# Kernel optimization log

Measured on AMD Instinct MI355X. Metric: run time of the kernel, lower is better.

The kernel has to match this reference:

```python
import jax, jax.numpy as jnp
import numpy as np

ALPHA = 0.5  # mixing weight between dot-product and wedge-norm terms


def setup_inputs() -> dict:
    key = jax.random.key(0)
    kq, kk, kv = jax.random.split(key, 3)
    B, L, H, E = 2, 2048, 8, 32
    queries = jax.random.normal(kq, (B, L, H, E), dtype=jnp.float32)
    keys = jax.random.normal(kk, (B, L, H, E), dtype=jnp.float32)
    values = jax.random.normal(kv, (B, L, H, E), dtype=jnp.float32)
    return {"queries": queries, "keys": keys, "values": values}


def reference(queries, keys, values):
    # queries: [B,L,H,E], keys: [B,S,H,E], values: [B,S,H,D]
    E = queries.shape[-1]
    scale = 1.0 / jnp.sqrt(jnp.asarray(E, dtype=queries.dtype))
    # dot product scores: [B,H,L,S]
    dot = jnp.einsum('blhe,bshe->bhls', queries, keys)
    # squared norms -> broadcastable [B,H,L,1] and [B,H,1,S]
    qn2 = jnp.sum(queries ** 2, axis=-1).transpose(0, 2, 1)[..., :, None]
    kn2 = jnp.sum(keys ** 2, axis=-1).transpose(0, 2, 1)[..., None, :]
    # wedge (Clifford) squared norm, clamped at 0
    wedge = jax.nn.relu(qn2 * kn2 - dot ** 2)
    scores = (ALPHA * dot - (1.0 - ALPHA) * wedge) * scale
    attn = jax.nn.softmax(scores, axis=-1)  # [B,H,L,S]
    # out: [B,L,H,D]
    out = jnp.einsum('bhls,bshd->blhd', attn, values)
    return out
```

## Files before the change

kernel.cpp:

```cpp
#include <hip/hip_runtime.h>
#include <hip/hip_bf16.h>
#include <math.h>


#define NB 2
#define NL 2048
#define NS 2048
#define NH 8
#define NBH 16
#define CSC 0.12751742f

#define WS_KN2_OFF 0u
#define WS_KHKL_OFF 131072u
#define WS_VT_OFF (131072u + 4194304u)
#define WS_PACC_OFF (131072u + 4194304u + 2097152u)
#define WS_PML_OFF (WS_PACC_OFF + 16777216u)
#define WS_NEED (WS_PML_OFF + 1048576u)

typedef float f32x4 __attribute__((ext_vector_type(4)));
typedef short s16x8 __attribute__((ext_vector_type(8)));
typedef unsigned short u16;

__device__ inline unsigned pk2(float a, float b) {
    __hip_bfloat162 t = __float22bfloat162_rn(make_float2(a, b));
    union { __hip_bfloat162 h; unsigned u; } cv;
    cv.h = t;
    return cv.u;
}
template <int CTRL>
__device__ inline float dpp_add(float x) {
    return x + __int_as_float(__builtin_amdgcn_mov_dpp(__float_as_int(x), CTRL, 0xF, 0xF, false));
}
__device__ inline void dma16(const void* gp, void* lp) {
    __builtin_amdgcn_global_load_lds(
        (__attribute__((address_space(1))) void*)(void*)gp,
        (__attribute__((address_space(3))) void*)lp, 16, 0, 0);
}
__device__ inline int swzK(int row) { return (row ^ (row >> 2)) & 3; }
__device__ inline int swzV(int row) { return (row + (row >> 3)) & 7; }

__global__ __launch_bounds__(256) void ga_pre(const float* __restrict__ K,
                                              const float* __restrict__ V,
                                              float* __restrict__ kn2w,
                                              u16* __restrict__ khkl,
                                              u16* __restrict__ vtw) {
    __shared__ float Vf[64][36];
    const int T = threadIdx.x;
    const int bh = blockIdx.x >> 5, stile = blockIdx.x & 31;
    const int b = bh >> 3, h = bh & 7;
    const int s0 = stile * 64;
    const int sk = T >> 2, kc = T & 3;

    const float* kp = K + ((size_t)((b * NS + s0 + sk) * NH + h)) * 32 + kc * 8;
    float4 f0 = *(const float4*)kp, f1 = *(const float4*)(kp + 4);
    float kx[8] = {f0.x, f0.y, f0.z, f0.w, f1.x, f1.y, f1.z, f1.w};
    unsigned hh[4], ll[4];
    float kn2p = 0.f;
#pragma unroll
    for (int i = 0; i < 4; i++) {
        float x0 = kx[2 * i], x1 = kx[2 * i + 1];
        kn2p = fmaf(x0, x0, kn2p);
        kn2p = fmaf(x1, x1, kn2p);
        unsigned h01 = pk2(x0, x1);
        hh[i] = h01;
        float h0 = __uint_as_float(h01 << 16);
        float h1 = __uint_as_float(h01 & 0xffff0000u);
        ll[i] = pk2(x0 - h0, x1 - h1);
    }
    u16* kd = khkl + ((size_t)(bh * NS + s0 + sk)) * 64;
    const int swk = sk & 7;
    *(uint4*)(kd + ((kc ^ swk) * 8)) = make_uint4(hh[0], hh[1], hh[2], hh[3]);
    *(uint4*)(kd + (((4 + kc) ^ swk) * 8)) = make_uint4(ll[0], ll[1], ll[2], ll[3]);
    kn2p = dpp_add<0xB1>(kn2p);
    kn2p = dpp_add<0x4E>(kn2p);
    if (kc == 0) kn2w[bh * NS + s0 + sk] = kn2p;

    const float* vp = V + ((size_t)((b * NS + s0 + sk) * NH + h)) * 32 + kc * 8;
    float4 g0 = *(const float4*)vp, g1 = *(const float4*)(vp + 4);
    *(float4*)&Vf[sk][kc * 8] = g0;
    *(float4*)&Vf[sk][kc * 8 + 4] = g1;
    __syncthreads();
    const int dr = T >> 3, c = T & 7;
    float vv[8];
#pragma unroll
    for (int i = 0; i < 8; i++) vv[i] = Vf[c * 8 + i][dr];
    const int phys = c ^ (dr & 7);
    *(uint4*)(vtw + ((size_t)(bh * 32 + dr)) * NS + s0 + phys * 8) =
        make_uint4(pk2(vv[0], vv[1]), pk2(vv[2], vv[3]), pk2(vv[4], vv[5]), pk2(vv[6], vv[7]));
}

__global__ __launch_bounds__(256, 4) void ga_dma(
    const float* __restrict__ Q, const float* __restrict__ kn2w,
    const u16* __restrict__ khkl, const u16* __restrict__ vtw,
    float* __restrict__ pacc, float* __restrict__ pml) {
    __shared__ u16 sK[2][64][64];
    __shared__ u16 sV[2][32][64];
    __shared__ u16 sP[4][16][64];

    const int T = threadIdx.x;
    const int lane = T & 63, wave = T >> 6;
    const int g = lane >> 4, lc = lane & 15, g8 = g * 8;
    const int blk = blockIdx.x;
    const int qt = blk & 31, strip = (blk >> 5) & 3, bh = blk >> 7;
    const int b = bh >> 3, h = bh & 7;
    const int qw = qt * 64 + wave * 16;
    const int kb0 = strip * 512;

    const float* qrow = Q + ((size_t)((b * NL + qw + lc) * NH + h)) * 32 + g8;
    float4 qa = *(const float4*)qrow, qb = *(const float4*)(qrow + 4);
    float q8[8] = {qa.x, qa.y, qa.z, qa.w, qb.x, qb.y, qb.z, qb.w};
    union { unsigned u4[4]; s16x8 v; } qh_, ql_;
    float qn2 = 0.f;
#pragma unroll
    for (int i = 0; i < 4; i++) {
        float x0 = q8[2 * i], x1 = q8[2 * i + 1];
        qn2 = fmaf(x0, x0, qn2);
        qn2 = fmaf(x1, x1, qn2);
        unsigned h01 = pk2(x0, x1);
        qh_.u4[i] = h01;
        float h0 = __uint_as_float(h01 << 16);
        float h1 = __uint_as_float(h01 & 0xffff0000u);
        ql_.u4[i] = pk2(x0 - h0, x1 - h1);
    }
    const s16x8 qh = qh_.v, ql = ql_.v;
    qn2 += __shfl_xor(qn2, 16);
    qn2 += __shfl_xor(qn2, 32);

    const char* ksrc = (const char*)khkl +
        ((size_t)(bh * NS + kb0 + 16 * wave)) * 128 + lane * 16;
    const char* vsrc = (const char*)vtw +
        ((size_t)(bh * 32 + 8 * wave + (lane >> 3))) * (NS * 2) +
        (size_t)(kb0 + (lane & 7) * 8) * 2;
    const float* kn2b = kn2w + (size_t)bh * NS + kb0;

    dma16(ksrc, &sK[0][16 * wave][0]);
    dma16(ksrc + 1024, &sK[0][16 * wave + 8][0]);
    dma16(vsrc, &sV[0][8 * wave][0]);
    __syncthreads();

    s16x8 ones;
#pragma unroll
    for (int i = 0; i < 8; i++) ones[i] = (short)0x3F80;

    f32x4 acc0 = {0.f, 0.f, 0.f, 0.f}, acc1 = {0.f, 0.f, 0.f, 0.f};
    float m = -1e30f, l = 0.f;
    const f32x4 z = {0.f, 0.f, 0.f, 0.f};
    const int sw = lc & 7;

    for (int t = 0; t < 8; ++t) {
        const int cur = t & 1;
        if (t + 1 < 8) {
            const char* k2 = ksrc + (size_t)(t + 1) * 8192;
            const char* v2 = vsrc + (size_t)(t + 1) * 128;
            dma16(k2, &sK[cur ^ 1][16 * wave][0]);
            dma16(k2 + 1024, &sK[cur ^ 1][16 * wave + 8][0]);
            dma16(v2, &sV[cur ^ 1][8 * wave][0]);
        }
        const int kl64 = t * 64;

        f32x4 d[4], kn2v[4];
#pragma unroll
        for (int st = 0; st < 4; st++) {
            kn2v[st] = *(const f32x4*)(kn2b + kl64 + 16 * st + 4 * g);
            s16x8 kh = *(s16x8*)&sK[cur][16 * st + lc][(g ^ sw) * 8];
            s16x8 klo = *(s16x8*)&sK[cur][16 * st + lc][((4 + g) ^ sw) * 8];
            f32x4 dd = __builtin_amdgcn_mfma_f32_16x16x32_bf16(klo, qh, z, 0, 0, 0);
            dd = __builtin_amdgcn_mfma_f32_16x16x32_bf16(kh, ql, dd, 0, 0, 0);
            dd = __builtin_amdgcn_mfma_f32_16x16x32_bf16(kh, qh, dd, 0, 0, 0);
            d[st] = dd;
        }
        s16x8 va0 = *(s16x8*)&sV[cur][lc][(g ^ sw) * 8];
        s16x8 va1 = *(s16x8*)&sV[cur][lc][((4 + g) ^ sw) * 8];
        s16x8 va2 = *(s16x8*)&sV[cur][lc + 16][(g ^ sw) * 8];
        s16x8 va3 = *(s16x8*)&sV[cur][lc + 16][((4 + g) ^ sw) * 8];

        float sc[4][4];
#pragma unroll
        for (int st = 0; st < 4; st++)
#pragma unroll
            for (int r = 0; r < 4; r++) {
                float dd = d[st][r];
                float c = qn2 * kn2v[st][r];
                sc[st][r] = fminf(dd, fmaf(dd, dd, -c) + dd);
            }

        float x0 = fmaxf(fmaxf(sc[0][0], sc[0][1]), fmaxf(sc[0][2], sc[0][3]));
        float x1 = fmaxf(fmaxf(sc[1][0], sc[1][1]), fmaxf(sc[1][2], sc[1][3]));
        float x2 = fmaxf(fmaxf(sc[2][0], sc[2][1]), fmaxf(sc[2][2], sc[2][3]));
        float x3 = fmaxf(fmaxf(sc[3][0], sc[3][1]), fmaxf(sc[3][2], sc[3][3]));
        float tm = fmaxf(fmaxf(x0, x1), fmaxf(x2, x3));
        tm = fmaxf(tm, __shfl_xor(tm, 16));
        tm = fmaxf(tm, __shfl_xor(tm, 32));
        const float nm = fmaxf(m, tm);
        const float negmC = -nm * CSC;
        const float al = __builtin_amdgcn_exp2f(fmaf(m, CSC, negmC));
        m = nm;
        float p[4][4];
#pragma unroll
        for (int st = 0; st < 4; st++)
#pragma unroll
            for (int r = 0; r < 4; r++)
                p[st][r] = __builtin_amdgcn_exp2f(fmaf(sc[st][r], CSC, negmC));

#pragma unroll
        for (int st = 0; st < 4; st++) {
            const int off = (((2 * st + (g >> 1)) ^ sw) << 3) + ((g & 1) << 2);
            *(uint2*)&sP[wave][lc][off] =
                make_uint2(pk2(p[st][0], p[st][1]), pk2(p[st][2], p[st][3]));
        }
        __builtin_amdgcn_s_waitcnt(0xC07F);
        s16x8 pb0 = *(s16x8*)&sP[wave][lc][(g ^ sw) * 8];
        s16x8 pb1 = *(s16x8*)&sP[wave][lc][((4 + g) ^ sw) * 8];

        acc0 *= al;
        acc1 *= al;
        acc0 = __builtin_amdgcn_mfma_f32_16x16x32_bf16(va0, pb0, acc0, 0, 0, 0);
        acc0 = __builtin_amdgcn_mfma_f32_16x16x32_bf16(va1, pb1, acc0, 0, 0, 0);
        acc1 = __builtin_amdgcn_mfma_f32_16x16x32_bf16(va2, pb0, acc1, 0, 0, 0);
        acc1 = __builtin_amdgcn_mfma_f32_16x16x32_bf16(va3, pb1, acc1, 0, 0, 0);
        f32x4 lt = __builtin_amdgcn_mfma_f32_16x16x32_bf16(ones, pb0, z, 0, 0, 0);
        lt = __builtin_amdgcn_mfma_f32_16x16x32_bf16(ones, pb1, lt, 0, 0, 0);
        l = fmaf(l, al, lt[0]);

        __syncthreads();
    }

    float* pa = pacc + (((size_t)bh * 4 + strip) * NL + (qw + lc)) * 32;
    *(f32x4*)(pa + 4 * g) = acc0;
    *(f32x4*)(pa + 16 + 4 * g) = acc1;
    if (g == 0) {
        *(float2*)(pml + (((size_t)bh * 4 + strip) * NL + (qw + lc)) * 2) =
            make_float2(m, l);
    }
}

__global__ __launch_bounds__(256) void ga_combine(const float* __restrict__ pacc,
                                                  const float* __restrict__ pml,
                                                  float* __restrict__ O) {
    const int tid = blockIdx.x * 256 + threadIdx.x;
    const int dq = tid & 7, q = (tid >> 3) & 2047, bh = tid >> 14;
    const int b = bh >> 3, h = bh & 7;
    float m[4], l[4];
#pragma unroll
    for (int s = 0; s < 4; s++) {
        float2 t = *(const float2*)(pml + (((size_t)bh * 4 + s) * NL + q) * 2);
        m[s] = t.x;
        l[s] = t.y;
    }
    float mf = fmaxf(fmaxf(m[0], m[1]), fmaxf(m[2], m[3]));
    float w[4], L = 0.f;
#pragma unroll
    for (int s = 0; s < 4; s++) {
        w[s] = __builtin_amdgcn_exp2f((m[s] - mf) * CSC);
        L = fmaf(l[s], w[s], L);
    }
    const float inv = 1.f / L;
    float4 o = make_float4(0.f, 0.f, 0.f, 0.f);
#pragma unroll
    for (int s = 0; s < 4; s++) {
        const float* pa = pacc + (((size_t)bh * 4 + s) * NL + q) * 32 + dq * 4;
        float4 a = *(const float4*)pa;
        o.x = fmaf(a.x, w[s], o.x);
        o.y = fmaf(a.y, w[s], o.y);
        o.z = fmaf(a.z, w[s], o.z);
        o.w = fmaf(a.w, w[s], o.w);
    }
    o.x *= inv; o.y *= inv; o.z *= inv; o.w *= inv;
    *(float4*)(O + (((size_t)(b * NL + q)) * NH + h) * 32 + dq * 4) = o;
}

__global__ __launch_bounds__(512, 4) void ga_fallback(
    const float* __restrict__ Q, const float* __restrict__ K,
    const float* __restrict__ V, float* __restrict__ O) {
    __shared__ union {
        struct {
            u16 Kh[2][64][32];
            u16 Kl[2][64][32];
            u16 Vt[2][32][64];
            float kn2[2][64];
        } s;
        struct { float acc[8][32][17]; float m[8][16]; float l[8][16]; } c;
    } u;
    __shared__ u16 sP[8][16][64];

    const int T = threadIdx.x;
    const int lane = T & 63, wave = T >> 6;
    const int g = lane >> 4, lc = lane & 15, g8 = g * 8;
    const int half = wave >> 2;
    const int qt = blockIdx.x & 31;
    const int bh = blockIdx.x >> 5;
    const int b = bh >> 3, h = bh & 7;
    const int qw = qt * 64 + (wave & 3) * 16;

    const float* qrow = Q + ((size_t)((b * NL + qw + lc) * NH + h)) * 32 + g8;
    float4 qa = *(const float4*)qrow, qb = *(const float4*)(qrow + 4);
    float q8[8] = {qa.x, qa.y, qa.z, qa.w, qb.x, qb.y, qb.z, qb.w};
    union { unsigned u4[4]; s16x8 v; } qh_, ql_;
    float qn2 = 0.f;
#pragma unroll
    for (int i = 0; i < 4; i++) {
        float x0 = q8[2 * i], x1 = q8[2 * i + 1];
        qn2 = fmaf(x0, x0, qn2);
        qn2 = fmaf(x1, x1, qn2);
        unsigned h01 = pk2(x0, x1);
        qh_.u4[i] = h01;
        float h0 = __uint_as_float(h01 << 16);
        float h1 = __uint_as_float(h01 & 0xffff0000u);
        ql_.u4[i] = pk2(x0 - h0, x1 - h1);
    }
    const s16x8 qh = qh_.v, ql = ql_.v;
    qn2 += __shfl_xor(qn2, 16);
    qn2 += __shfl_xor(qn2, 32);

    const int Tl = T & 255;
    const int sk = Tl >> 2, kc = Tl & 3;
    const int dv = Tl & 31, vc = Tl >> 5;
    const float* kbase = K + ((size_t)(b * NS * NH) + h) * 32;
    const float* vbase = V + ((size_t)(b * NS * NH) + h) * 32;
    const int kphys = (kc ^ swzK(sk)) * 8;
    const int vphys = (vc ^ swzV(dv)) * 8;

    int s0 = half * 1024;
    float4 ka = *(const float4*)(kbase + (size_t)(s0 + sk) * 256 + kc * 8);
    float4 kb = *(const float4*)(kbase + (size_t)(s0 + sk) * 256 + kc * 8 + 4);
    float vr[8];
#pragma unroll
    for (int i = 0; i < 8; i++) vr[i] = vbase[(size_t)(s0 + 8 * vc + i) * 256 + dv];

    f32x4 acc0 = {0.f, 0.f, 0.f, 0.f}, acc1 = {0.f, 0.f, 0.f, 0.f};
    float m = -INFINITY, l = 0.f;

    for (int t = 0; t < 16; ++t) {
        {
            float kx[8] = {ka.x, ka.y, ka.z, ka.w, kb.x, kb.y, kb.z, kb.w};
            unsigned hh[4], ll[4];
            float kn2p = 0.f;
#pragma unroll
            for (int i = 0; i < 4; i++) {
                float x0 = kx[2 * i], x1 = kx[2 * i + 1];
                kn2p = fmaf(x0, x0, kn2p);
                kn2p = fmaf(x1, x1, kn2p);
                unsigned h01 = pk2(x0, x1);
                hh[i] = h01;
                float h0 = __uint_as_float(h01 << 16);
                float h1 = __uint_as_float(h01 & 0xffff0000u);
                ll[i] = pk2(x0 - h0, x1 - h1);
            }
            *(uint4*)&u.s.Kh[half][sk][kphys] = make_uint4(hh[0], hh[1], hh[2], hh[3]);
            *(uint4*)&u.s.Kl[half][sk][kphys] = make_uint4(ll[0], ll[1], ll[2], ll[3]);
            kn2p = dpp_add<0xB1>(kn2p);
            kn2p = dpp_add<0x4E>(kn2p);
            if (kc == 0) u.s.kn2[half][sk] = kn2p;
            *(uint4*)&u.s.Vt[half][dv][vphys] =
                make_uint4(pk2(vr[0], vr[1]), pk2(vr[2], vr[3]),
                           pk2(vr[4], vr[5]), pk2(vr[6], vr[7]));
        }
        const int tn = (t + 1 < 16) ? t + 1 : t;
        const int sn = half * 1024 + tn * 64;
        ka = *(const float4*)(kbase + (size_t)(sn + sk) * 256 + kc * 8);
        kb = *(const float4*)(kbase + (size_t)(sn + sk) * 256 + kc * 8 + 4);
#pragma unroll
        for (int i = 0; i < 8; i++) vr[i] = vbase[(size_t)(sn + 8 * vc + i) * 256 + dv];

        __syncthreads();

        f32x4 d[4], kn2v[4];
        const f32x4 z = {0.f, 0.f, 0.f, 0.f};
        const int skr = swzK(lc);
#pragma unroll
        for (int st = 0; st < 4; st++) {
            kn2v[st] = *(f32x4*)&u.s.kn2[half][16 * st + 4 * g];
            s16x8 kh = *(s16x8*)&u.s.Kh[half][16 * st + lc][(g ^ skr) * 8];
            s16x8 kl = *(s16x8*)&u.s.Kl[half][16 * st + lc][(g ^ skr) * 8];
            f32x4 dd = __builtin_amdgcn_mfma_f32_16x16x32_bf16(kl, qh, z, 0, 0, 0);
            dd = __builtin_amdgcn_mfma_f32_16x16x32_bf16(kh, ql, dd, 0, 0, 0);
            dd = __builtin_amdgcn_mfma_f32_16x16x32_bf16(kh, qh, dd, 0, 0, 0);
            d[st] = dd;
        }

        float sc[4][4];
#pragma unroll
        for (int st = 0; st < 4; st++)
#pragma unroll
            for (int r = 0; r < 4; r++) {
                float dd = d[st][r];
                float w = fmaxf(fmaf(-dd, dd, qn2 * kn2v[st][r]), 0.f);
                sc[st][r] = (dd - w) * CSC;
            }

        float x0 = fmaxf(fmaxf(sc[0][0], sc[0][1]), fmaxf(sc[0][2], sc[0][3]));
        float x1 = fmaxf(fmaxf(sc[1][0], sc[1][1]), fmaxf(sc[1][2], sc[1][3]));
        float x2 = fmaxf(fmaxf(sc[2][0], sc[2][1]), fmaxf(sc[2][2], sc[2][3]));
        float x3 = fmaxf(fmaxf(sc[3][0], sc[3][1]), fmaxf(sc[3][2], sc[3][3]));
        float tm = fmaxf(fmaxf(x0, x1), fmaxf(x2, x3));
        tm = fmaxf(tm, __shfl_xor(tm, 16));
        tm = fmaxf(tm, __shfl_xor(tm, 32));
        const float nm = fmaxf(m, tm);
        const float al = __builtin_amdgcn_exp2f(m - nm);
        m = nm;
        float p[4][4], ls = 0.f;
#pragma unroll
        for (int st = 0; st < 4; st++)
#pragma unroll
            for (int r = 0; r < 4; r++) {
                p[st][r] = __builtin_amdgcn_exp2f(sc[st][r] - nm);
                ls += p[st][r];
            }
        l = fmaf(l, al, ls);
        acc0 *= al;
        acc1 *= al;

#pragma unroll
        for (int st = 0; st < 4; st++) {
            const int off = ((2 * st + (g >> 1)) ^ (lc & 7)) * 8 + (g & 1) * 4;
            *(uint2*)&sP[wave][lc][off] =
                make_uint2(pk2(p[st][0], p[st][1]), pk2(p[st][2], p[st][3]));
        }
        __builtin_amdgcn_s_waitcnt(0xC07F);

        const int svl = swzV(lc), svh = swzV(lc + 16), spl = lc & 7;
        s16x8 va00 = *(s16x8*)&u.s.Vt[half][lc][(g ^ svl) * 8];
        s16x8 va01 = *(s16x8*)&u.s.Vt[half][lc][((4 + g) ^ svl) * 8];
        s16x8 va10 = *(s16x8*)&u.s.Vt[half][lc + 16][(g ^ svh) * 8];
        s16x8 va11 = *(s16x8*)&u.s.Vt[half][lc + 16][((4 + g) ^ svh) * 8];
        s16x8 pb0 = *(s16x8*)&sP[wave][lc][(g ^ spl) * 8];
        s16x8 pb1 = *(s16x8*)&sP[wave][lc][((4 + g) ^ spl) * 8];
        acc0 = __builtin_amdgcn_mfma_f32_16x16x32_bf16(va00, pb0, acc0, 0, 0, 0);
        acc0 = __builtin_amdgcn_mfma_f32_16x16x32_bf16(va01, pb1, acc0, 0, 0, 0);
        acc1 = __builtin_amdgcn_mfma_f32_16x16x32_bf16(va10, pb0, acc1, 0, 0, 0);
        acc1 = __builtin_amdgcn_mfma_f32_16x16x32_bf16(va11, pb1, acc1, 0, 0, 0);

        __syncthreads();
    }

    l += __shfl_xor(l, 16);
    l += __shfl_xor(l, 32);
#pragma unroll
    for (int r = 0; r < 4; r++) {
        u.c.acc[wave][4 * g + r][lc] = acc0[r];
        u.c.acc[wave][16 + 4 * g + r][lc] = acc1[r];
    }
    if (lane < 16) {
        u.c.m[wave][lc] = m;
        u.c.l[wave][lc] = l;
    }
    __syncthreads();

    const int q = T >> 3, dq = (T & 7) * 4, qr = q & 15;
    const int w0 = q >> 4, w1 = w0 + 4;
    float m0 = u.c.m[w0][qr], m1 = u.c.m[w1][qr];
    float l0 = u.c.l[w0][qr], l1 = u.c.l[w1][qr];
    float mf = fmaxf(m0, m1);
    float e0 = __builtin_amdgcn_exp2f(m0 - mf);
    float e1 = __builtin_amdgcn_exp2f(m1 - mf);
    float inv = 1.f / fmaf(l1, e1, l0 * e0);
    e0 *= inv;
    e1 *= inv;
    float4 o;
    o.x = u.c.acc[w0][dq + 0][qr] * e0 + u.c.acc[w1][dq + 0][qr] * e1;
    o.y = u.c.acc[w0][dq + 1][qr] * e0 + u.c.acc[w1][dq + 1][qr] * e1;
    o.z = u.c.acc[w0][dq + 2][qr] * e0 + u.c.acc[w1][dq + 2][qr] * e1;
    o.w = u.c.acc[w0][dq + 3][qr] * e0 + u.c.acc[w1][dq + 3][qr] * e1;
    *(float4*)(O + ((size_t)((b * NL + qt * 64 + q) * NH + h)) * 32 + dq) = o;
}

extern "C" void kernel_launch(void* const* d_in, const int* in_sizes, int n_in,
                              void* d_out, int out_size, void* d_ws, size_t ws_size,
                              hipStream_t stream) {
    const float* Q = (const float*)d_in[0];
    const float* K = (const float*)d_in[1];
    const float* V = (const float*)d_in[2];
    float* O = (float*)d_out;

    if (ws_size >= (size_t)WS_NEED) {
        float* kn2w = (float*)((char*)d_ws + WS_KN2_OFF);
        u16* khkl = (u16*)((char*)d_ws + WS_KHKL_OFF);
        u16* vtw = (u16*)((char*)d_ws + WS_VT_OFF);
        float* pacc = (float*)((char*)d_ws + WS_PACC_OFF);
        float* pml = (float*)((char*)d_ws + WS_PML_OFF);
        ga_pre<<<NBH * 32, 256, 0, stream>>>(K, V, kn2w, khkl, vtw);
        ga_dma<<<NBH * 32 * 4, 256, 0, stream>>>(Q, kn2w, khkl, vtw, pacc, pml);
        ga_combine<<<(NBH * NL * 8) / 256, 256, 0, stream>>>(pacc, pml, O);
    } else {
        ga_fallback<<<NBH * 32, 512, 0, stream>>>(Q, K, V, O);
    }
}
```

Baseline: 106.2 us.

## Halve KV strips, defer softmax rescale, permlane-swap P, prefetch kn2

Reduces the split-KV factor from 4 strips to 2, so each workgroup handles 16 tiles and the partial-accumulator workspace and combine pass shrink. The running max is now updated only when a tile's max exceeds the current max by more than a threshold (a lazy rescale). The LDS round trip for P is replaced by in-register v_permlane32/16 swaps, and kn2 loads are prefetched one tile ahead. Fewer strips lowers grid parallelism (1024 blocks instead of 2048), and the deferred rescale relies on bounded exponent growth for fp32/bf16 accuracy.

Result: no change. 105.1 us (-1.0%).

```diff
diff --git a/kernel.cpp b/kernel.cpp
--- a/kernel.cpp
+++ b/kernel.cpp
@@ -8,14 +8,17 @@
 #define NS 2048
 #define NH 8
 #define NBH 16
+#define STRIPS 2
+#define NT 16
 #define CSC 0.12751742f
+#define DEFER_THR 24.0f
 
 #define WS_KN2_OFF 0u
 #define WS_KHKL_OFF 131072u
 #define WS_VT_OFF (131072u + 4194304u)
 #define WS_PACC_OFF (131072u + 4194304u + 2097152u)
-#define WS_PML_OFF (WS_PACC_OFF + 16777216u)
-#define WS_NEED (WS_PML_OFF + 1048576u)
+#define WS_PML_OFF (WS_PACC_OFF + 8388608u)
+#define WS_NEED (WS_PML_OFF + 524288u)
 
 typedef float f32x4 __attribute__((ext_vector_type(4)));
 typedef short s16x8 __attribute__((ext_vector_type(8)));
@@ -35,6 +38,12 @@
     __builtin_amdgcn_global_load_lds(
         (__attribute__((address_space(1))) void*)(void*)gp,
         (__attribute__((address_space(3))) void*)lp, 16, 0, 0);
+}
+__device__ inline void pl32(unsigned& a, unsigned& b) {
+    asm("v_permlane32_swap_b32 %0, %1" : "+v"(a), "+v"(b));
+}
+__device__ inline void pl16(unsigned& a, unsigned& b) {
+    asm("v_permlane16_swap_b32 %0, %1" : "+v"(a), "+v"(b));
 }
 __device__ inline int swzK(int row) { return (row ^ (row >> 2)) & 3; }
 __device__ inline int swzV(int row) { return (row + (row >> 3)) & 7; }
@@ -95,16 +104,15 @@
     float* __restrict__ pacc, float* __restrict__ pml) {
     __shared__ u16 sK[2][64][64];
     __shared__ u16 sV[2][32][64];
-    __shared__ u16 sP[4][16][64];
 
     const int T = threadIdx.x;
     const int lane = T & 63, wave = T >> 6;
     const int g = lane >> 4, lc = lane & 15, g8 = g * 8;
     const int blk = blockIdx.x;
-    const int qt = blk & 31, strip = (blk >> 5) & 3, bh = blk >> 7;
+    const int qt = blk & 31, strip = (blk >> 5) & 1, bh = blk >> 6;
     const int b = bh >> 3, h = bh & 7;
     const int qw = qt * 64 + wave * 16;
-    const int kb0 = strip * 512;
+    const int kb0 = strip * 1024;
 
     const float* qrow = Q + ((size_t)((b * NL + qw + lc) * NH + h)) * 32 + g8;
     float4 qa = *(const float4*)qrow, qb = *(const float4*)(qrow + 4);
@@ -136,6 +144,11 @@
     dma16(ksrc, &sK[0][16 * wave][0]);
     dma16(ksrc + 1024, &sK[0][16 * wave + 8][0]);
     dma16(vsrc, &sV[0][8 * wave][0]);
+
+    f32x4 kn2v[4], kn2n[4];
+#pragma unroll
+    for (int st = 0; st < 4; st++) kn2v[st] = *(const f32x4*)(kn2b + 16 * st + 4 * g);
+
     __syncthreads();
 
     s16x8 ones;
@@ -147,21 +160,22 @@
     const f32x4 z = {0.f, 0.f, 0.f, 0.f};
     const int sw = lc & 7;
 
-    for (int t = 0; t < 8; ++t) {
+    for (int t = 0; t < NT; ++t) {
         const int cur = t & 1;
-        if (t + 1 < 8) {
+        if (t + 1 < NT) {
             const char* k2 = ksrc + (size_t)(t + 1) * 8192;
             const char* v2 = vsrc + (size_t)(t + 1) * 128;
             dma16(k2, &sK[cur ^ 1][16 * wave][0]);
             dma16(k2 + 1024, &sK[cur ^ 1][16 * wave + 8][0]);
             dma16(v2, &sV[cur ^ 1][8 * wave][0]);
-        }
-        const int kl64 = t * 64;
-
-        f32x4 d[4], kn2v[4];
+#pragma unroll
+            for (int st = 0; st < 4; st++)
+                kn2n[st] = *(const f32x4*)(kn2b + (t + 1) * 64 + 16 * st + 4 * g);
+        }
+
+        f32x4 d[4];
 #pragma unroll
         for (int st = 0; st < 4; st++) {
-            kn2v[st] = *(const f32x4*)(kn2b + kl64 + 16 * st + 4 * g);
             s16x8 kh = *(s16x8*)&sK[cur][16 * st + lc][(g ^ sw) * 8];
             s16x8 klo = *(s16x8*)&sK[cur][16 * st + lc][((4 + g) ^ sw) * 8];
             f32x4 dd = __builtin_amdgcn_mfma_f32_16x16x32_bf16(klo, qh, z, 0, 0, 0);
@@ -189,12 +203,17 @@
         float x2 = fmaxf(fmaxf(sc[2][0], sc[2][1]), fmaxf(sc[2][2], sc[2][3]));
         float x3 = fmaxf(fmaxf(sc[3][0], sc[3][1]), fmaxf(sc[3][2], sc[3][3]));
         float tm = fmaxf(fmaxf(x0, x1), fmaxf(x2, x3));
-        tm = fmaxf(tm, __shfl_xor(tm, 16));
-        tm = fmaxf(tm, __shfl_xor(tm, 32));
-        const float nm = fmaxf(m, tm);
-        const float negmC = -nm * CSC;
-        const float al = __builtin_amdgcn_exp2f(fmaf(m, CSC, negmC));
-        m = nm;
+        if (!__all(tm <= m + DEFER_THR)) {
+            tm = fmaxf(tm, __shfl_xor(tm, 16));
+            tm = fmaxf(tm, __shfl_xor(tm, 32));
+            const float nm = fmaxf(m, tm);
+            const float al = __builtin_amdgcn_exp2f((m - nm) * CSC);
+            m = nm;
+            acc0 *= al;
+            acc1 *= al;
+            l *= al;
+        }
+        const float negmC = -m * CSC;
         float p[4][4];
 #pragma unroll
         for (int st = 0; st < 4; st++)
@@ -202,34 +221,39 @@
             for (int r = 0; r < 4; r++)
                 p[st][r] = __builtin_amdgcn_exp2f(fmaf(sc[st][r], CSC, negmC));
 
-#pragma unroll
-        for (int st = 0; st < 4; st++) {
-            const int off = (((2 * st + (g >> 1)) ^ sw) << 3) + ((g & 1) << 2);
-            *(uint2*)&sP[wave][lc][off] =
-                make_uint2(pk2(p[st][0], p[st][1]), pk2(p[st][2], p[st][3]));
-        }
-        __builtin_amdgcn_s_waitcnt(0xC07F);
-        s16x8 pb0 = *(s16x8*)&sP[wave][lc][(g ^ sw) * 8];
-        s16x8 pb1 = *(s16x8*)&sP[wave][lc][((4 + g) ^ sw) * 8];
-
-        acc0 *= al;
-        acc1 *= al;
+        unsigned w00 = pk2(p[0][0], p[0][1]), w01 = pk2(p[0][2], p[0][3]);
+        unsigned w10 = pk2(p[1][0], p[1][1]), w11 = pk2(p[1][2], p[1][3]);
+        unsigned w20 = pk2(p[2][0], p[2][1]), w21 = pk2(p[2][2], p[2][3]);
+        unsigned w30 = pk2(p[3][0], p[3][1]), w31 = pk2(p[3][2], p[3][3]);
+        pl32(w00, w10); pl32(w01, w11);
+        pl16(w00, w10); pl16(w01, w11);
+        pl32(w20, w30); pl32(w21, w31);
+        pl16(w20, w30); pl16(w21, w31);
+        union { uint4 u; s16x8 v; } Pb0, Pb1;
+        Pb0.u = make_uint4(w00, w01, w10, w11);
+        Pb1.u = make_uint4(w20, w21, w30, w31);
+        const s16x8 pb0 = Pb0.v, pb1 = Pb1.v;
+
         acc0 = __builtin_amdgcn_mfma_f32_16x16x32_bf16(va0, pb0, acc0, 0, 0, 0);
         acc0 = __builtin_amdgcn_mfma_f32_16x16x32_bf16(va1, pb1, acc0, 0, 0, 0);
         acc1 = __builtin_amdgcn_mfma_f32_16x16x32_bf16(va2, pb0, acc1, 0, 0, 0);
         acc1 = __builtin_amdgcn_mfma_f32_16x16x32_bf16(va3, pb1, acc1, 0, 0, 0);
         f32x4 lt = __builtin_amdgcn_mfma_f32_16x16x32_bf16(ones, pb0, z, 0, 0, 0);
         lt = __builtin_amdgcn_mfma_f32_16x16x32_bf16(ones, pb1, lt, 0, 0, 0);
-        l = fmaf(l, al, lt[0]);
-
+        l += lt[0];
+
+        if (t + 1 < NT) {
+#pragma unroll
+            for (int st = 0; st < 4; st++) kn2v[st] = kn2n[st];
+        }
         __syncthreads();
     }
 
-    float* pa = pacc + (((size_t)bh * 4 + strip) * NL + (qw + lc)) * 32;
+    float* pa = pacc + (((size_t)bh * STRIPS + strip) * NL + (qw + lc)) * 32;
     *(f32x4*)(pa + 4 * g) = acc0;
     *(f32x4*)(pa + 16 + 4 * g) = acc1;
     if (g == 0) {
-        *(float2*)(pml + (((size_t)bh * 4 + strip) * NL + (qw + lc)) * 2) =
+        *(float2*)(pml + (((size_t)bh * STRIPS + strip) * NL + (qw + lc)) * 2) =
             make_float2(m, l);
     }
 }
@@ -240,32 +264,22 @@
     const int tid = blockIdx.x * 256 + threadIdx.x;
     const int dq = tid & 7, q = (tid >> 3) & 2047, bh = tid >> 14;
     const int b = bh >> 3, h = bh & 7;
-    float m[4], l[4];
-#pragma unroll
-    for (int s = 0; s < 4; s++) {
-        float2 t = *(const float2*)(pml + (((size_t)bh * 4 + s) * NL + q) * 2);
-        m[s] = t.x;
-        l[s] = t.y;
-    }
-    float mf = fmaxf(fmaxf(m[0], m[1]), fmaxf(m[2], m[3]));
-    float w[4], L = 0.f;
-#pragma unroll
-    for (int s = 0; s < 4; s++) {
-        w[s] = __builtin_amdgcn_exp2f((m[s] - mf) * CSC);
-        L = fmaf(l[s], w[s], L);
-    }
-    const float inv = 1.f / L;
-    float4 o = make_float4(0.f, 0.f, 0.f, 0.f);
-#pragma unroll
-    for (int s = 0; s < 4; s++) {
-        const float* pa = pacc + (((size_t)bh * 4 + s) * NL + q) * 32 + dq * 4;
-        float4 a = *(const float4*)pa;
-        o.x = fmaf(a.x, w[s], o.x);
-        o.y = fmaf(a.y, w[s], o.y);
-        o.z = fmaf(a.z, w[s], o.z);
-        o.w = fmaf(a.w, w[s], o.w);
-    }
-    o.x *= inv; o.y *= inv; o.z *= inv; o.w *= inv;
+    float2 t0 = *(const float2*)(pml + (((size_t)bh * STRIPS + 0) * NL + q) * 2);
+    float2 t1 = *(const float2*)(pml + (((size_t)bh * STRIPS + 1) * NL + q) * 2);
+    const float mf = fmaxf(t0.x, t1.x);
+    float w0 = __builtin_amdgcn_exp2f((t0.x - mf) * CSC);
+    float w1 = __builtin_amdgcn_exp2f((t1.x - mf) * CSC);
+    const float inv = 1.f / fmaf(t0.y, w0, t1.y * w1);
+    w0 *= inv;
+    w1 *= inv;
+    const float* pa0 = pacc + (((size_t)bh * STRIPS + 0) * NL + q) * 32 + dq * 4;
+    const float* pa1 = pacc + (((size_t)bh * STRIPS + 1) * NL + q) * 32 + dq * 4;
+    float4 a0 = *(const float4*)pa0, a1 = *(const float4*)pa1;
+    float4 o;
+    o.x = fmaf(a0.x, w0, a1.x * w1);
+    o.y = fmaf(a0.y, w0, a1.y * w1);
+    o.z = fmaf(a0.z, w0, a1.z * w1);
+    o.w = fmaf(a0.w, w0, a1.w * w1);
     *(float4*)(O + (((size_t)(b * NL + q)) * NH + h) * 32 + dq * 4) = o;
 }
 
@@ -479,7 +493,7 @@
         float* pacc = (float*)((char*)d_ws + WS_PACC_OFF);
         float* pml = (float*)((char*)d_ws + WS_PML_OFF);
         ga_pre<<<NBH * 32, 256, 0, stream>>>(K, V, kn2w, khkl, vtw);
-        ga_dma<<<NBH * 32 * 4, 256, 0, stream>>>(Q, kn2w, khkl, vtw, pacc, pml);
+        ga_dma<<<NBH * 32 * STRIPS, 256, 0, stream>>>(Q, kn2w, khkl, vtw, pacc, pml);
         ga_combine<<<(NBH * NL * 8) / 256, 256, 0, stream>>>(pacc, pml, O);
     } else {
         ga_fallback<<<NBH * 32, 512, 0, stream>>>(Q, K, V, O);
```

## Process two query tiles per wave, defer max rescale, permlane P transpose

Applied to the files above, without the earlier changes.

Each wave now handles two 16-row query tiles against the same K/V tile held in LDS. This halves K/V loads and DMA per query and halves the grid size. The P matrix is rearranged for the PV MFMA with permlane16/32 swaps in registers instead of a round trip through LDS. The online-softmax max update is skipped unless some score exceeds the running max by a threshold. Row sums now accumulate through a ones-MFMA, score math uses packed float2 ops, and ga_pre gets an LDS swizzle for the V transpose. In exchange, register pressure rises (launch bounds drop from 4 to 3 blocks per SM), the grid is smaller, and deferring the rescale lets exponent values grow up to the threshold.

Result: no change. 105.0 us (-1.1%).

```diff
diff --git a/kernel.cpp b/kernel.cpp
--- a/kernel.cpp
+++ b/kernel.cpp
@@ -8,7 +8,10 @@
 #define NS 2048
 #define NH 8
 #define NBH 16
+#define STRIPS 4
+#define NT 8
 #define CSC 0.12751742f
+#define DEFER_THR 24.0f
 
 #define WS_KN2_OFF 0u
 #define WS_KHKL_OFF 131072u
@@ -18,6 +21,7 @@
 #define WS_NEED (WS_PML_OFF + 1048576u)
 
 typedef float f32x4 __attribute__((ext_vector_type(4)));
+typedef float f32x2 __attribute__((ext_vector_type(2)));
 typedef short s16x8 __attribute__((ext_vector_type(8)));
 typedef unsigned short u16;
 
@@ -35,6 +39,12 @@
     __builtin_amdgcn_global_load_lds(
         (__attribute__((address_space(1))) void*)(void*)gp,
         (__attribute__((address_space(3))) void*)lp, 16, 0, 0);
+}
+__device__ inline void pl32(unsigned& a, unsigned& b) {
+    asm("v_permlane32_swap_b32 %0, %1" : "+v"(a), "+v"(b));
+}
+__device__ inline void pl16(unsigned& a, unsigned& b) {
+    asm("v_permlane16_swap_b32 %0, %1" : "+v"(a), "+v"(b));
 }
 __device__ inline int swzK(int row) { return (row ^ (row >> 2)) & 3; }
 __device__ inline int swzV(int row) { return (row + (row >> 3)) & 7; }
@@ -77,61 +87,90 @@
 
     const float* vp = V + ((size_t)((b * NS + s0 + sk) * NH + h)) * 32 + kc * 8;
     float4 g0 = *(const float4*)vp, g1 = *(const float4*)(vp + 4);
-    *(float4*)&Vf[sk][kc * 8] = g0;
-    *(float4*)&Vf[sk][kc * 8 + 4] = g1;
+    const int chv = kc ^ ((sk >> 3) & 3);
+    *(float4*)&Vf[sk][chv * 8] = g0;
+    *(float4*)&Vf[sk][chv * 8 + 4] = g1;
     __syncthreads();
     const int dr = T >> 3, c = T & 7;
     float vv[8];
 #pragma unroll
-    for (int i = 0; i < 8; i++) vv[i] = Vf[c * 8 + i][dr];
+    for (int i = 0; i < 8; i++)
+        vv[i] = Vf[c * 8 + i][(((dr >> 3) ^ (c & 3)) << 3) + (dr & 7)];
     const int phys = c ^ (dr & 7);
     *(uint4*)(vtw + ((size_t)(bh * 32 + dr)) * NS + s0 + phys * 8) =
         make_uint4(pk2(vv[0], vv[1]), pk2(vv[2], vv[3]), pk2(vv[4], vv[5]), pk2(vv[6], vv[7]));
 }
 
-__global__ __launch_bounds__(256, 4) void ga_dma(
+__global__ __launch_bounds__(256, 3) void ga_dma(
     const float* __restrict__ Q, const float* __restrict__ kn2w,
     const u16* __restrict__ khkl, const u16* __restrict__ vtw,
     float* __restrict__ pacc, float* __restrict__ pml) {
     __shared__ u16 sK[2][64][64];
     __shared__ u16 sV[2][32][64];
-    __shared__ u16 sP[4][16][64];
 
     const int T = threadIdx.x;
     const int lane = T & 63, wave = T >> 6;
     const int g = lane >> 4, lc = lane & 15, g8 = g * 8;
     const int blk = blockIdx.x;
-    const int qt = blk & 31, strip = (blk >> 5) & 3, bh = blk >> 7;
+    const int qt = blk & 15, strip = (blk >> 4) & 3, bh = blk >> 6;
     const int b = bh >> 3, h = bh & 7;
-    const int qw = qt * 64 + wave * 16;
+    const int qwa = qt * 128 + wave * 16;
+    const int qwb = qwa + 64;
     const int kb0 = strip * 512;
 
-    const float* qrow = Q + ((size_t)((b * NL + qw + lc) * NH + h)) * 32 + g8;
-    float4 qa = *(const float4*)qrow, qb = *(const float4*)(qrow + 4);
-    float q8[8] = {qa.x, qa.y, qa.z, qa.w, qb.x, qb.y, qb.z, qb.w};
-    union { unsigned u4[4]; s16x8 v; } qh_, ql_;
-    float qn2 = 0.f;
-#pragma unroll
-    for (int i = 0; i < 4; i++) {
-        float x0 = q8[2 * i], x1 = q8[2 * i + 1];
-        qn2 = fmaf(x0, x0, qn2);
-        qn2 = fmaf(x1, x1, qn2);
-        unsigned h01 = pk2(x0, x1);
-        qh_.u4[i] = h01;
-        float h0 = __uint_as_float(h01 << 16);
-        float h1 = __uint_as_float(h01 & 0xffff0000u);
-        ql_.u4[i] = pk2(x0 - h0, x1 - h1);
-    }
-    const s16x8 qh = qh_.v, ql = ql_.v;
-    qn2 += __shfl_xor(qn2, 16);
-    qn2 += __shfl_xor(qn2, 32);
+    s16x8 qha, qla, qhb, qlb;
+    float qn2a, qn2b;
+    {
+        const float* qrow = Q + ((size_t)((b * NL + qwa + lc) * NH + h)) * 32 + g8;
+        float4 qa = *(const float4*)qrow, qb = *(const float4*)(qrow + 4);
+        float q8[8] = {qa.x, qa.y, qa.z, qa.w, qb.x, qb.y, qb.z, qb.w};
+        union { unsigned u4[4]; s16x8 v; } qh_, ql_;
+        float qn2 = 0.f;
+#pragma unroll
+        for (int i = 0; i < 4; i++) {
+            float x0 = q8[2 * i], x1 = q8[2 * i + 1];
+            qn2 = fmaf(x0, x0, qn2);
+            qn2 = fmaf(x1, x1, qn2);
+            unsigned h01 = pk2(x0, x1);
+            qh_.u4[i] = h01;
+            float h0 = __uint_as_float(h01 << 16);
+            float h1 = __uint_as_float(h01 & 0xffff0000u);
+            ql_.u4[i] = pk2(x0 - h0, x1 - h1);
+        }
+        qha = qh_.v; qla = ql_.v;
+        qn2 += __shfl_xor(qn2, 16);
+        qn2 += __shfl_xor(qn2, 32);
+        qn2a = qn2;
+    }
+    {
+        const float* qrow = Q + ((size_t)((b * NL + qwb + lc) * NH + h)) * 32 + g8;
+        float4 qa = *(const float4*)qrow, qb = *(const float4*)(qrow + 4);
+        float q8[8] = {qa.x, qa.y, qa.z, qa.w, qb.x, qb.y, qb.z, qb.w};
+        union { unsigned u4[4]; s16x8 v; } qh_, ql_;
+        float qn2 = 0.f;
+#pragma unroll
+        for (int i = 0; i < 4; i++) {
+            float x0 = q8[2 * i], x1 = q8[2 * i + 1];
+            qn2 = fmaf(x0, x0, qn2);
+            qn2 = fmaf(x1, x1, qn2);
+            unsigned h01 = pk2(x0, x1);
+            qh_.u4[i] = h01;
+            float h0 = __uint_as_float(h01 << 16);
+            float h1 = __uint_as_float(h01 & 0xffff0000u);
+            ql_.u4[i] = pk2(x0 - h0, x1 - h1);
+        }
+        qhb = qh_.v; qlb = ql_.v;
+        qn2 += __shfl_xor(qn2, 16);
+        qn2 += __shfl_xor(qn2, 32);
+        qn2b = qn2;
+    }
 
     const char* ksrc = (const char*)khkl +
         ((size_t)(bh * NS + kb0 + 16 * wave)) * 128 + lane * 16;
     const char* vsrc = (const char*)vtw +
         ((size_t)(bh * 32 + 8 * wave + (lane >> 3))) * (NS * 2) +
         (size_t)(kb0 + (lane & 7) * 8) * 2;
-    const float* kn2b = kn2w + (size_t)bh * NS + kb0;
+    const float* kn2b = kn2w + (size_t)bh * NS + kb0 + 4 * g;
 
     dma16(ksrc, &sK[0][16 * wave][0]);
     dma16(ksrc + 1024, &sK[0][16 * wave + 8][0]);
@@ -142,95 +181,166 @@
 #pragma unroll
     for (int i = 0; i < 8; i++) ones[i] = (short)0x3F80;
 
-    f32x4 acc0 = {0.f, 0.f, 0.f, 0.f}, acc1 = {0.f, 0.f, 0.f, 0.f};
-    float m = -1e30f, l = 0.f;
+    f32x4 acc0a = {0.f, 0.f, 0.f, 0.f}, acc1a = {0.f, 0.f, 0.f, 0.f};
+    f32x4 acc0b = {0.f, 0.f, 0.f, 0.f}, acc1b = {0.f, 0.f, 0.f, 0.f};
+    f32x4 lacca = {0.f, 0.f, 0.f, 0.f}, laccb = {0.f, 0.f, 0.f, 0.f};
+    float ma = -1e30f, mb = -1e30f;
     const f32x4 z = {0.f, 0.f, 0.f, 0.f};
     const int sw = lc & 7;
 
-    for (int t = 0; t < 8; ++t) {
+#pragma unroll 1
+    for (int t = 0; t < NT; ++t) {
         const int cur = t & 1;
-        if (t + 1 < 8) {
+        if (t + 1 < NT) {
             const char* k2 = ksrc + (size_t)(t + 1) * 8192;
             const char* v2 = vsrc + (size_t)(t + 1) * 128;
             dma16(k2, &sK[cur ^ 1][16 * wave][0]);
             dma16(k2 + 1024, &sK[cur ^ 1][16 * wave + 8][0]);
             dma16(v2, &sV[cur ^ 1][8 * wave][0]);
         }
-        const int kl64 = t * 64;
-
-        f32x4 d[4], kn2v[4];
+
+        f32x4 da[4], db[4], kn2m[4];
 #pragma unroll
         for (int st = 0; st < 4; st++) {
-            kn2v[st] = *(const f32x4*)(kn2b + kl64 + 16 * st + 4 * g);
+            kn2m[st] = *(const f32x4*)(kn2b + t * 64 + 16 * st);
             s16x8 kh = *(s16x8*)&sK[cur][16 * st + lc][(g ^ sw) * 8];
             s16x8 klo = *(s16x8*)&sK[cur][16 * st + lc][((4 + g) ^ sw) * 8];
-            f32x4 dd = __builtin_amdgcn_mfma_f32_16x16x32_bf16(klo, qh, z, 0, 0, 0);
-            dd = __builtin_amdgcn_mfma_f32_16x16x32_bf16(kh, ql, dd, 0, 0, 0);
-            dd = __builtin_amdgcn_mfma_f32_16x16x32_bf16(kh, qh, dd, 0, 0, 0);
-            d[st] = dd;
+            f32x4 dd = __builtin_amdgcn_mfma_f32_16x16x32_bf16(klo, qha, z, 0, 0, 0);
+            dd = __builtin_amdgcn_mfma_f32_16x16x32_bf16(kh, qla, dd, 0, 0, 0);
+            da[st] = __builtin_amdgcn_mfma_f32_16x16x32_bf16(kh, qha, dd, 0, 0, 0);
+            f32x4 de = __builtin_amdgcn_mfma_f32_16x16x32_bf16(klo, qhb, z, 0, 0, 0);
+            de = __builtin_amdgcn_mfma_f32_16x16x32_bf16(kh, qlb, de, 0, 0, 0);
+            db[st] = __builtin_amdgcn_mfma_f32_16x16x32_bf16(kh, qhb, de, 0, 0, 0);
         }
         s16x8 va0 = *(s16x8*)&sV[cur][lc][(g ^ sw) * 8];
         s16x8 va1 = *(s16x8*)&sV[cur][lc][((4 + g) ^ sw) * 8];
         s16x8 va2 = *(s16x8*)&sV[cur][lc + 16][(g ^ sw) * 8];
         s16x8 va3 = *(s16x8*)&sV[cur][lc + 16][((4 + g) ^ sw) * 8];
 
-        float sc[4][4];
-#pragma unroll
-        for (int st = 0; st < 4; st++)
-#pragma unroll
-            for (int r = 0; r < 4; r++) {
-                float dd = d[st][r];
-                float c = qn2 * kn2v[st][r];
-                sc[st][r] = fminf(dd, fmaf(dd, dd, -c) + dd);
+        float sca[4][4], scb[4][4];
+        {
+            const f32x2 qa2 = {qn2a, qn2a}, qb2 = {qn2b, qn2b};
+#pragma unroll
+            for (int st = 0; st < 4; st++) {
+                f32x2 kk0 = {kn2m[st][0], kn2m[st][1]}, kk1 = {kn2m[st][2], kn2m[st][3]};
+                f32x2 dd0 = {da[st][0], da[st][1]}, dd1 = {da[st][2], da[st][3]};
+                f32x2 e0 = dd0 - qa2 * kk0;
+                f32x2 e1 = dd1 - qa2 * kk1;
+                f32x2 t0 = dd0 * dd0 + e0;
+                f32x2 t1 = dd1 * dd1 + e1;
+                sca[st][0] = fminf(da[st][0], t0[0]);
+                sca[st][1] = fminf(da[st][1], t0[1]);
+                sca[st][2] = fminf(da[st][2], t1[0]);
+                sca[st][3] = fminf(da[st][3], t1[1]);
+                f32x2 ee0 = {db[st][0], db[st][1]}, ee1 = {db[st][2], db[st][3]};
+                f32x2 f0 = ee0 - qb2 * kk0;
+                f32x2 f1 = ee1 - qb2 * kk1;
+                f32x2 u0 = ee0 * ee0 + f0;
+                f32x2 u1 = ee1 * ee1 + f1;
+                scb[st][0] = fminf(db[st][0], u0[0]);
+                scb[st][1] = fminf(db[st][1], u0[1]);
+                scb[st][2] = fminf(db[st][2], u1[0]);
+                scb[st][3] = fminf(db[st][3], u1[1]);
             }
-
-        float x0 = fmaxf(fmaxf(sc[0][0], sc[0][1]), fmaxf(sc[0][2], sc[0][3]));
-        float x1 = fmaxf(fmaxf(sc[1][0], sc[1][1]), fmaxf(sc[1][2], sc[1][3]));
-        float x2 = fmaxf(fmaxf(sc[2][0], sc[2][1]), fmaxf(sc[2][2], sc[2][3]));
-        float x3 = fmaxf(fmaxf(sc[3][0], sc[3][1]), fmaxf(sc[3][2], sc[3][3]));
-        float tm = fmaxf(fmaxf(x0, x1), fmaxf(x2, x3));
-        tm = fmaxf(tm, __shfl_xor(tm, 16));
-        tm = fmaxf(tm, __shfl_xor(tm, 32));
-        const float nm = fmaxf(m, tm);
-        const float negmC = -nm * CSC;
-        const float al = __builtin_amdgcn_exp2f(fmaf(m, CSC, negmC));
-        m = nm;
-        float p[4][4];
-#pragma unroll
-        for (int st = 0; st < 4; st++)
-#pragma unroll
-            for (int r = 0; r < 4; r++)
-                p[st][r] = __builtin_amdgcn_exp2f(fmaf(sc[st][r], CSC, negmC));
-
+        }
+
+        float a0 = fmaxf(fmaxf(sca[0][0], sca[0][1]), fmaxf(sca[0][2], sca[0][3]));
+        float a1 = fmaxf(fmaxf(sca[1][0], sca[1][1]), fmaxf(sca[1][2], sca[1][3]));
+        float a2 = fmaxf(fmaxf(sca[2][0], sca[2][1]), fmaxf(sca[2][2], sca[2][3]));
+        float a3 = fmaxf(fmaxf(sca[3][0], sca[3][1]), fmaxf(sca[3][2], sca[3][3]));
+        float tma = fmaxf(fmaxf(a0, a1), fmaxf(a2, a3));
+        float b0 = fmaxf(fmaxf(scb[0][0], scb[0][1]), fmaxf(scb[0][2], scb[0][3]));
+        float b1 = fmaxf(fmaxf(scb[1][0], scb[1][1]), fmaxf(scb[1][2], scb[1][3]));
+        float b2 = fmaxf(fmaxf(scb[2][0], scb[2][1]), fmaxf(scb[2][2], scb[2][3]));
+        float b3 = fmaxf(fmaxf(scb[3][0], scb[3][1]), fmaxf(scb[3][2], scb[3][3]));
+        float tmb = fmaxf(fmaxf(b0, b1), fmaxf(b2, b3));
+        if (!__all((tma <= ma + DEFER_THR) && (tmb <= mb + DEFER_THR))) {
+            tma = fmaxf(tma, __shfl_xor(tma, 16));
+            tma = fmaxf(tma, __shfl_xor(tma, 32));
+            tmb = fmaxf(tmb, __shfl_xor(tmb, 16));
+            tmb = fmaxf(tmb, __shfl_xor(tmb, 32));
+            const float nma = fmaxf(ma, tma), nmb = fmaxf(mb, tmb);
+            const float ala = __builtin_amdgcn_exp2f((ma - nma) * CSC);
+            const float alb = __builtin_amdgcn_exp2f((mb - nmb) * CSC);
+            ma = nma; mb = nmb;
+            acc0a *= ala; acc1a *= ala; lacca *= ala;
+            acc0b *= alb; acc1b *= alb; laccb *= alb;
+        }
+        const float negmaC = -ma * CSC, negmbC = -mb * CSC;
+        const f32x2 cscv = {CSC, CSC};
+        const f32x2 nmav = {negmaC, negmaC}, nmbv = {negmbC, negmbC};
+        float pa[4][4], pb[4][4];
 #pragma unroll
         for (int st = 0; st < 4; st++) {
-            const int off = (((2 * st + (g >> 1)) ^ sw) << 3) + ((g & 1) << 2);
-            *(uint2*)&sP[wave][lc][off] =
-                make_uint2(pk2(p[st][0], p[st][1]), pk2(p[st][2], p[st][3]));
-        }
-        __builtin_amdgcn_s_waitcnt(0xC07F);
-        s16x8 pb0 = *(s16x8*)&sP[wave][lc][(g ^ sw) * 8];
-        s16x8 pb1 = *(s16x8*)&sP[wave][lc][((4 + g) ^ sw) * 8];
-
-        acc0 *= al;
-        acc1 *= al;
-        acc0 = __builtin_amdgcn_mfma_f32_16x16x32_bf16(va0, pb0, acc0, 0, 0, 0);
-        acc0 = __builtin_amdgcn_mfma_f32_16x16x32_bf16(va1, pb1, acc0, 0, 0, 0);
-        acc1 = __builtin_amdgcn_mfma_f32_16x16x32_bf16(va2, pb0, acc1, 0, 0, 0);
-        acc1 = __builtin_amdgcn_mfma_f32_16x16x32_bf16(va3, pb1, acc1, 0, 0, 0);
-        f32x4 lt = __builtin_amdgcn_mfma_f32_16x16x32_bf16(ones, pb0, z, 0, 0, 0);
-        lt = __builtin_amdgcn_mfma_f32_16x16x32_bf16(ones, pb1, lt, 0, 0, 0);
-        l = fmaf(l, al, lt[0]);
+            f32x2 s0 = {sca[st][0], sca[st][1]}, s1 = {sca[st][2], sca[st][3]};
+            f32x2 e0 = s0 * cscv + nmav;
+            f32x2 e1 = s1 * cscv + nmav;
+            pa[st][0] = __builtin_amdgcn_exp2f(e0[0]);
+            pa[st][1] = __builtin_amdgcn_exp2f(e0[1]);
+            pa[st][2] = __builtin_amdgcn_exp2f(e1[0]);
+            pa[st][3] = __builtin_amdgcn_exp2f(e1[1]);
+            f32x2 u0 = {scb[st][0], scb[st][1]}, u1 = {scb[st][2], scb[st][3]};
+            f32x2 f0 = u0 * cscv + nmbv;
+            f32x2 f1 = u1 * cscv + nmbv;
+            pb[st][0] = __builtin_amdgcn_exp2f(f0[0]);
+            pb[st][1] = __builtin_amdgcn_exp2f(f0[1]);
+            pb[st][2] = __builtin_amdgcn_exp2f(f1[0]);
+            pb[st][3] = __builtin_amdgcn_exp2f(f1[1]);
+        }
+
+        {
+            unsigned w00 = pk2(pa[0][0], pa[0][1]), w01 = pk2(pa[0][2], pa[0][3]);
+            unsigned w10 = pk2(pa[1][0], pa[1][1]), w11 = pk2(pa[1][2], pa[1][3]);
+            unsigned w20 = pk2(pa[2][0], pa[2][1]), w21 = pk2(pa[2][2], pa[2][3]);
+            unsigned w30 = pk2(pa[3][0], pa[3][1]), w31 = pk2(pa[3][2], pa[3][3]);
+            pl32(w00, w10); pl32(w01, w11);
+            pl16(w00, w10); pl16(w01, w11);
+            pl32(w20, w30); pl32(w21, w31);
+            pl16(w20, w30); pl16(w21, w31);
+            union { uint4 u; s16x8 v; } P0, P1;
+            P0.u = make_uint4(w00, w01, w10, w11);
+            P1.u = make_uint4(w20, w21, w30, w31);
+            acc0a = __builtin_amdgcn_mfma_f32_16x16x32_bf16(va0, P0.v, acc0a, 0, 0, 0);
+            acc0a = __builtin_amdgcn_mfma_f32_16x16x32_bf16(va1, P1.v, acc0a, 0, 0, 0);
+            acc1a = __builtin_amdgcn_mfma_f32_16x16x32_bf16(va2, P0.v, acc1a, 0, 0, 0);
+            acc1a = __builtin_amdgcn_mfma_f32_16x16x32_bf16(va3, P1.v, acc1a, 0, 0, 0);
+            lacca = __builtin_amdgcn_mfma_f32_16x16x32_bf16(ones, P0.v, lacca, 0, 0, 0);
+            lacca = __builtin_amdgcn_mfma_f32_16x16x32_bf16(ones, P1.v, lacca, 0, 0, 0);
+        }
+        {
+            unsigned w00 = pk2(pb[0][0], pb[0][1]), w01 = pk2(pb[0][2], pb[0][3]);
+            unsigned w10 = pk2(pb[1][0], pb[1][1]), w11 = pk2(pb[1][2], pb[1][3]);
+            unsigned w20 = pk2(pb[2][0], pb[2][1]), w21 = pk2(pb[2][2], pb[2][3]);
+            unsigned w30 = pk2(pb[3][0], pb[3][1]), w31 = pk2(pb[3][2], pb[3][3]);
+            pl32(w00, w10); pl32(w01, w11);
+            pl16(w00, w10); pl16(w01, w11);
+            pl32(w20, w30); pl32(w21, w31);
+            pl16(w20, w30); pl16(w21, w31);
+            union { uint4 u; s16x8 v; } P0, P1;
+            P0.u = make_uint4(w00, w01, w10, w11);
+            P1.u = make_uint4(w20, w21, w30, w31);
+            acc0b = __builtin_amdgcn_mfma_f32_16x16x32_bf16(va0, P0.v, acc0b, 0, 0, 0);
+            acc0b = __builtin_amdgcn_mfma_f32_16x16x32_bf16(va1, P1.v, acc0b, 0, 0, 0);
+            acc1b = __builtin_amdgcn_mfma_f32_16x16x32_bf16(va2, P0.v, acc1b, 0, 0, 0);
+            acc1b = __builtin_amdgcn_mfma_f32_16x16x32_bf16(va3, P1.v, acc1b, 0, 0, 0);
+            laccb = __builtin_amdgcn_mfma_f32_16x16x32_bf16(ones, P0.v, laccb, 0, 0, 0);
+            laccb = __builtin_amdgcn_mfma_f32_16x16x32_bf16(ones, P1.v, laccb, 0, 0, 0);
+        }
 
         __syncthreads();
     }
 
-    float* pa = pacc + (((size_t)bh * 4 + strip) * NL + (qw + lc)) * 32;
-    *(f32x4*)(pa + 4 * g) = acc0;
-    *(f32x4*)(pa + 16 + 4 * g) = acc1;
+    float* paa = pacc + (((size_t)bh * STRIPS + strip) * NL + (qwa + lc)) * 32;
+    *(f32x4*)(paa + 4 * g) = acc0a;
+    *(f32x4*)(paa + 16 + 4 * g) = acc1a;
+    float* pab = pacc + (((size_t)bh * STRIPS + strip) * NL + (qwb + lc)) * 32;
+    *(f32x4*)(pab + 4 * g) = acc0b;
+    *(f32x4*)(pab + 16 + 4 * g) = acc1b;
     if (g == 0) {
-        *(float2*)(pml + (((size_t)bh * 4 + strip) * NL + (qw + lc)) * 2) =
-            make_float2(m, l);
+        *(float2*)(pml + (((size_t)bh * STRIPS + strip) * NL + (qwa + lc)) * 2) =
+            make_float2(ma, lacca[0]);
+        *(float2*)(pml + (((size_t)bh * STRIPS + strip) * NL + (qwb + lc)) * 2) =
+            make_float2(mb, laccb[0]);
     }
 }
 
@@ -243,7 +353,7 @@
     float m[4], l[4];
 #pragma unroll
     for (int s = 0; s < 4; s++) {
-        float2 t = *(const float2*)(pml + (((size_t)bh * 4 + s) * NL + q) * 2);
+        float2 t = *(const float2*)(pml + (((size_t)bh * STRIPS + s) * NL + q) * 2);
         m[s] = t.x;
         l[s] = t.y;
     }
@@ -258,7 +368,7 @@
     float4 o = make_float4(0.f, 0.f, 0.f, 0.f);
 #pragma unroll
     for (int s = 0; s < 4; s++) {
-        const float* pa = pacc + (((size_t)bh * 4 + s) * NL + q) * 32 + dq * 4;
+        const float* pa = pacc + (((size_t)bh * STRIPS + s) * NL + q) * 32 + dq * 4;
         float4 a = *(const float4*)pa;
         o.x = fmaf(a.x, w[s], o.x);
         o.y = fmaf(a.y, w[s], o.y);
@@ -479,7 +589,7 @@
         float* pacc = (float*)((char*)d_ws + WS_PACC_OFF);
         float* pml = (float*)((char*)d_ws + WS_PML_OFF);
         ga_pre<<<NBH * 32, 256, 0, stream>>>(K, V, kn2w, khkl, vtw);
-        ga_dma<<<NBH * 32 * 4, 256, 0, stream>>>(Q, kn2w, khkl, vtw, pacc, pml);
+        ga_dma<<<NBH * 16 * STRIPS, 256, 0, stream>>>(Q, kn2w, khkl, vtw, pacc, pml);
         ga_combine<<<(NBH * NL * 8) / 256, 256, 0, stream>>>(pacc, pml, O);
     } else {
         ga_fallback<<<NBH * 32, 512, 0, stream>>>(Q, K, V, O);
```
